# Optimization experiments

Measured on AMD Instinct MI355X. Metric: run time of the kernel, lower is better.

The kernel has to match this reference:

```python
import jax, jax.numpy as jnp
import numpy as np


def setup_inputs() -> dict:
    key = jax.random.key(0)
    k1, k2, k3, k4 = jax.random.split(key, 4)
    n, m = 4096, 1024  # n video frames, 1024-d features
    scale = 0.02
    return {
        "x": jax.random.normal(k1, (n, m), dtype=jnp.float32),
        "WQ": jax.random.normal(k2, (m, m), dtype=jnp.float32) * scale,  # torch Linear weight [out,in]
        "WK": jax.random.normal(k3, (m, m), dtype=jnp.float32) * scale,
        "WV": jax.random.normal(k4, (m, m), dtype=jnp.float32) * scale,
    }


def _quaternion_logits(q, k):
    """Hamilton-product attention logits: 4 tensors of shape [Lq, Lk]."""
    qr, qx, qy, qz = jnp.split(q, 4, axis=-1)
    kr, kx, ky, kz = jnp.split(k, 4, axis=-1)
    dot = lambda a, b: jnp.einsum('qd,kd->qk', a, b)
    r = dot(qr, kr) - dot(qx, kx) - dot(qy, ky) - dot(qz, kz)
    i = dot(qr, kx) + dot(qx, kr) + dot(qy, kz) - dot(qz, ky)
    j = dot(qr, ky) - dot(qx, kz) + dot(qy, kr) + dot(qz, kx)
    kk = dot(qr, kz) + dot(qx, ky) - dot(qy, kx) + dot(qz, kr)
    return [r, i, j, kk]


def reference(x, WQ, WK, WV):
    # QKV projections (torch Linear, no bias): y = x @ W.T
    Q = x @ WQ.T
    K = x @ WK.T
    V = x @ WV.T
    v_vals = jnp.split(V, 4, axis=-1)  # 4 chunks of depth d/4 (tensor2tensor quaternion attn)
    logits = _quaternion_logits(Q, K)
    outs = []
    w = None
    for l, v in zip(logits, v_vals):
        w = jax.nn.softmax(l, axis=-1)  # per-component softmax over keys
        outs.append(w @ v)
    y = jnp.concatenate(outs, axis=-1)  # [n, d]
    # original returns the attention weights from the last component (loop-leaked var)
    return y, w
```

## Files before the change

kernel.cpp:

```cpp
#include <hip/hip_runtime.h>
#include <cmath>

typedef __attribute__((ext_vector_type(8))) short short8;
typedef __attribute__((ext_vector_type(8))) unsigned short ushort8_t;
typedef __attribute__((ext_vector_type(8))) _Float16 half8;
typedef __attribute__((ext_vector_type(4))) float f32x4;
typedef unsigned short u16;

__device__ __forceinline__ u16 f2h(float f) {
    _Float16 h = (_Float16)f;
    return __builtin_bit_cast(u16, h);
}
__device__ __forceinline__ float h2f(u16 b) {
    return (float)__builtin_bit_cast(_Float16, b);
}

#define GLD16(g, l)                                                              \
    __builtin_amdgcn_global_load_lds(                                            \
        (const __attribute__((address_space(1))) unsigned int*)(g),              \
        (__attribute__((address_space(3))) unsigned int*)(l), 16, 0, 0)

#define MFMA_F16(a, b, c)                                                        \
    __builtin_amdgcn_mfma_f32_16x16x32_f16(                                      \
        __builtin_bit_cast(half8, (a)), __builtin_bit_cast(half8, (b)), (c), 0, 0, 0)
#define SBAR() asm volatile("s_barrier" ::: "memory")

__global__ __launch_bounds__(256) void to_h_all(
    const float* __restrict__ x, const float* __restrict__ WQ,
    const float* __restrict__ WK, const float* __restrict__ WV,
    u16* __restrict__ xh, u16* __restrict__ Wh)
{
    int bid = blockIdx.x;
    const float* src;
    u16* dst;
    int off;
    if (bid < 4096) { src = x; dst = xh; off = bid; }
    else {
        int j = bid - 4096;
        int wsel = j >> 10;
        off = j & 1023;
        src = wsel == 0 ? WQ : (wsel == 1 ? WK : WV);
        dst = Wh + (size_t)wsel * 1024 * 1024;
    }
    int idx = off * 256 + threadIdx.x;
    float4 v = reinterpret_cast<const float4*>(src)[idx];
    ushort4 h;
    h.x = f2h(v.x); h.y = f2h(v.y); h.z = f2h(v.z); h.w = f2h(v.w);
    reinterpret_cast<ushort4*>(dst)[idx] = h;
}

__global__ __launch_bounds__(512, 2) void logits8(
    const u16* __restrict__ A, const u16* __restrict__ B, const u16* __restrict__ Bneg,
    u16* __restrict__ P, float* __restrict__ pm, float* __restrict__ ps,
    int perm_packed, int sign_packed)
{
    constexpr int NT = 16;
    __shared__ u16 L[2][2][256 * 64];
    const int tid = threadIdx.x;
    const int l = tid & 63, w = tid >> 6;
    const int wr = w >> 2, wc = w & 3;
    const int lr = l & 15, lh = l >> 4;
    const int bid = (int)blockIdx.x;
    const int xcd = bid & 7, idx = bid >> 3;
    const int rowp = (xcd >> 1) * 4 + (idx >> 3);
    const int colp = (xcd & 1) * 8 + (idx & 7);
    const int row0 = rowp * 256, col0 = colp * 256;
    const int srow = l >> 3;
    const int scol = ((l & 7) ^ (l >> 3)) * 8;

    f32x4 acc[8][4] = {};

    auto stage = [&](int t) {
        int kA = t * 64;
        int ch = kA >> 8;
        int p = (perm_packed >> (2 * ch)) & 3;
        const u16* Bsrc = ((sign_packed >> ch) & 1) ? Bneg : B;
        int kB = (p << 8) + (kA & 255);
        int bf = t & 1;
        #pragma unroll
        for (int i = 0; i < 4; ++i) {
            int r0 = w * 32 + i * 8;
            GLD16(&A[(size_t)(row0 + r0 + srow) * 1024 + kA + scol], &L[bf][0][r0 * 64]);
        }
        #pragma unroll
        for (int i = 0; i < 4; ++i) {
            int r0 = w * 32 + i * 8;
            GLD16(&Bsrc[(size_t)(col0 + r0 + srow) * 1024 + kB + scol], &L[bf][1][r0 * 64]);
        }
    };
    auto readA = [&](int bf, int m, int kh) -> short8 {
        int row = wr * 128 + m * 16 + lr;
        int c = ((kh * 4 + lh) ^ (lr & 7)) * 8;
        return *reinterpret_cast<const short8*>(&L[bf][0][row * 64 + c]);
    };
    auto readB = [&](int bf, int n, int kh) -> short8 {
        int row = wc * 64 + n * 16 + lr;
        int c = ((kh * 4 + lh) ^ (lr & 7)) * 8;
        return *reinterpret_cast<const short8*>(&L[bf][1][row * 64 + c]);
    };

    stage(0);
    stage(1);
    asm volatile("s_waitcnt vmcnt(8)" ::: "memory");
    SBAR();

    #pragma unroll 2
    for (int t = 0; t < NT; ++t) {
        const int bf = t & 1;
        short8 am[4][2], bn[4][2];
        #pragma unroll
        for (int m = 0; m < 4; ++m) { am[m][0] = readA(bf, m, 0); am[m][1] = readA(bf, m, 1); }
        #pragma unroll
        for (int n = 0; n < 2; ++n) { bn[n][0] = readB(bf, n, 0); bn[n][1] = readB(bf, n, 1); }
        SBAR();
        __builtin_amdgcn_s_setprio(1);
        #pragma unroll
        for (int m = 0; m < 4; ++m)
            #pragma unroll
            for (int n = 0; n < 2; ++n) {
                acc[m][n] = MFMA_F16(am[m][0], bn[n][0], acc[m][n]);
                acc[m][n] = MFMA_F16(am[m][1], bn[n][1], acc[m][n]);
            }
        __builtin_amdgcn_s_setprio(0);
        SBAR();
        #pragma unroll
        for (int n = 2; n < 4; ++n) { bn[n][0] = readB(bf, n, 0); bn[n][1] = readB(bf, n, 1); }
        SBAR();
        __builtin_amdgcn_s_setprio(1);
        #pragma unroll
        for (int m = 0; m < 4; ++m)
            #pragma unroll
            for (int n = 2; n < 4; ++n) {
                acc[m][n] = MFMA_F16(am[m][0], bn[n][0], acc[m][n]);
                acc[m][n] = MFMA_F16(am[m][1], bn[n][1], acc[m][n]);
            }
        __builtin_amdgcn_s_setprio(0);
        SBAR();
        #pragma unroll
        for (int m = 0; m < 4; ++m) { am[m][0] = readA(bf, 4 + m, 0); am[m][1] = readA(bf, 4 + m, 1); }
        SBAR();
        __builtin_amdgcn_s_setprio(1);
        #pragma unroll
        for (int m = 0; m < 4; ++m)
            #pragma unroll
            for (int n = 2; n < 4; ++n) {
                acc[4 + m][n] = MFMA_F16(am[m][0], bn[n][0], acc[4 + m][n]);
                acc[4 + m][n] = MFMA_F16(am[m][1], bn[n][1], acc[4 + m][n]);
            }
        __builtin_amdgcn_s_setprio(0);
        SBAR();
        if (t + 2 < NT) stage(t + 2);
        SBAR();
        __builtin_amdgcn_s_setprio(1);
        #pragma unroll
        for (int m = 0; m < 4; ++m)
            #pragma unroll
            for (int n = 0; n < 2; ++n) {
                acc[4 + m][n] = MFMA_F16(am[m][0], bn[n][0], acc[4 + m][n]);
                acc[4 + m][n] = MFMA_F16(am[m][1], bn[n][1], acc[4 + m][n]);
            }
        __builtin_amdgcn_s_setprio(0);
        if (t + 2 < NT) { asm volatile("s_waitcnt vmcnt(8)" ::: "memory"); }
        else           { asm volatile("s_waitcnt vmcnt(0)" ::: "memory"); }
        SBAR();
    }

    const int tcol = (col0 >> 6) + wc;
    float* T = reinterpret_cast<float*>(&L[0][0][0]) + w * 1088;
    const int rq = l >> 2;
    const int cq = l & 3;
    #pragma unroll
    for (int m = 0; m < 8; ++m) {
        #pragma unroll
        for (int n = 0; n < 4; ++n)
            #pragma unroll
            for (int j = 0; j < 4; ++j)
                T[(lh * 4 + j) * 68 + n * 16 + lr] = acc[m][n][j];
        float vals[16];
        #pragma unroll
        for (int q = 0; q < 4; ++q) {
            f32x4 v4 = *reinterpret_cast<const f32x4*>(&T[rq * 68 + cq * 16 + q * 4]);
            vals[q * 4 + 0] = v4[0]; vals[q * 4 + 1] = v4[1];
            vals[q * 4 + 2] = v4[2]; vals[q * 4 + 3] = v4[3];
        }
        float mx = vals[0];
        #pragma unroll
        for (int c = 1; c < 16; ++c) mx = fmaxf(mx, vals[c]);
        mx = fmaxf(mx, __shfl_xor(mx, 1, 64));
        mx = fmaxf(mx, __shfl_xor(mx, 2, 64));
        float e[16];
        float s = 0.f;
        #pragma unroll
        for (int c = 0; c < 16; ++c) { e[c] = expf(vals[c] - mx); s += e[c]; }
        s += __shfl_xor(s, 1, 64);
        s += __shfl_xor(s, 2, 64);
        int row = row0 + wr * 128 + m * 16 + rq;
        if (cq == 0) {
            pm[(size_t)row * 64 + tcol] = mx;
            ps[(size_t)row * 64 + tcol] = s;
        }
        ushort8_t d0, d1;
        #pragma unroll
        for (int c = 0; c < 8; ++c) d0[c] = f2h(e[c]);
        #pragma unroll
        for (int c = 0; c < 8; ++c) d1[c] = f2h(e[c + 8]);
        size_t go = (size_t)row * 4096 + col0 + wc * 64 + cq * 16;
        *reinterpret_cast<ushort8_t*>(&P[go]) = d0;
        *reinterpret_cast<ushort8_t*>(&P[go + 8]) = d1;
    }
}

__global__ __launch_bounds__(512, 2) void qkv8(
    const u16* __restrict__ A, const u16* __restrict__ B,
    u16* __restrict__ Qh, u16* __restrict__ Kh, u16* __restrict__ Khn,
    u16* __restrict__ Vt)
{
    constexpr int NT = 16;
    __shared__ u16 L[2][2][256 * 64];
    const int tid = threadIdx.x;
    const int l = tid & 63, w = tid >> 6;
    const int wr = w >> 2, wc = w & 3;
    const int lr = l & 15, lh = l >> 4;
    const int bid = (int)blockIdx.x;
    const int wgid = (bid & 7) * 24 + (bid >> 3);
    const int row0 = (wgid / 12) * 256, col0 = (wgid % 12) * 256;
    const int srow = l >> 3;
    const int scol = ((l & 7) ^ (l >> 3)) * 8;

    f32x4 acc[8][4] = {};

    auto stage = [&](int t) {
        int k0 = t * 64;
        int bf = t & 1;
        #pragma unroll
        for (int i = 0; i < 4; ++i) {
            int r0 = w * 32 + i * 8;
            GLD16(&A[(size_t)(row0 + r0 + srow) * 1024 + k0 + scol], &L[bf][0][r0 * 64]);
        }
        #pragma unroll
        for (int i = 0; i < 4; ++i) {
            int r0 = w * 32 + i * 8;
            GLD16(&B[(size_t)(col0 + r0 + srow) * 1024 + k0 + scol], &L[bf][1][r0 * 64]);
        }
    };
    auto readA = [&](int bf, int m, int kh) -> short8 {
        int row = wr * 128 + m * 16 + lr;
        int c = ((kh * 4 + lh) ^ (lr & 7)) * 8;
        return *reinterpret_cast<const short8*>(&L[bf][0][row * 64 + c]);
    };
    auto readB = [&](int bf, int n, int kh) -> short8 {
        int row = wc * 64 + n * 16 + lr;
        int c = ((kh * 4 + lh) ^ (lr & 7)) * 8;
        return *reinterpret_cast<const short8*>(&L[bf][1][row * 64 + c]);
    };

    stage(0);
    stage(1);
    asm volatile("s_waitcnt vmcnt(8)" ::: "memory");
    SBAR();

    #pragma unroll 2
    for (int t = 0; t < NT; ++t) {
        const int bf = t & 1;
        short8 am[4][2], bn[4][2];
        #pragma unroll
        for (int m = 0; m < 4; ++m) { am[m][0] = readA(bf, m, 0); am[m][1] = readA(bf, m, 1); }
        #pragma unroll
        for (int n = 0; n < 2; ++n) { bn[n][0] = readB(bf, n, 0); bn[n][1] = readB(bf, n, 1); }
        SBAR();
        __builtin_amdgcn_s_setprio(1);
        #pragma unroll
        for (int m = 0; m < 4; ++m)
            #pragma unroll
            for (int n = 0; n < 2; ++n) {
                acc[m][n] = MFMA_F16(am[m][0], bn[n][0], acc[m][n]);
                acc[m][n] = MFMA_F16(am[m][1], bn[n][1], acc[m][n]);
            }
        __builtin_amdgcn_s_setprio(0);
        SBAR();
        #pragma unroll
        for (int n = 2; n < 4; ++n) { bn[n][0] = readB(bf, n, 0); bn[n][1] = readB(bf, n, 1); }
        SBAR();
        __builtin_amdgcn_s_setprio(1);
        #pragma unroll
        for (int m = 0; m < 4; ++m)
            #pragma unroll
            for (int n = 2; n < 4; ++n) {
                acc[m][n] = MFMA_F16(am[m][0], bn[n][0], acc[m][n]);
                acc[m][n] = MFMA_F16(am[m][1], bn[n][1], acc[m][n]);
            }
        __builtin_amdgcn_s_setprio(0);
        SBAR();
        #pragma unroll
        for (int m = 0; m < 4; ++m) { am[m][0] = readA(bf, 4 + m, 0); am[m][1] = readA(bf, 4 + m, 1); }
        SBAR();
        __builtin_amdgcn_s_setprio(1);
        #pragma unroll
        for (int m = 0; m < 4; ++m)
            #pragma unroll
            for (int n = 2; n < 4; ++n) {
                acc[4 + m][n] = MFMA_F16(am[m][0], bn[n][0], acc[4 + m][n]);
                acc[4 + m][n] = MFMA_F16(am[m][1], bn[n][1], acc[4 + m][n]);
            }
        __builtin_amdgcn_s_setprio(0);
        SBAR();
        if (t + 2 < NT) stage(t + 2);
        SBAR();
        __builtin_amdgcn_s_setprio(1);
        #pragma unroll
        for (int m = 0; m < 4; ++m)
            #pragma unroll
            for (int n = 0; n < 2; ++n) {
                acc[4 + m][n] = MFMA_F16(am[m][0], bn[n][0], acc[4 + m][n]);
                acc[4 + m][n] = MFMA_F16(am[m][1], bn[n][1], acc[4 + m][n]);
            }
        __builtin_amdgcn_s_setprio(0);
        if (t + 2 < NT) { asm volatile("s_waitcnt vmcnt(8)" ::: "memory"); }
        else           { asm volatile("s_waitcnt vmcnt(0)" ::: "memory"); }
        SBAR();
    }

    const int mode = col0 >> 10;
    #pragma unroll
    for (int m = 0; m < 8; ++m)
        #pragma unroll
        for (int n = 0; n < 4; ++n) {
            int gr = row0 + wr * 128 + m * 16 + lh * 4;
            int gc = col0 + wc * 64 + n * 16 + lr;
            int gcl = gc & 1023;
            f32x4 v = acc[m][n];
            if (mode == 0) {
                #pragma unroll
                for (int j = 0; j < 4; ++j)
                    Qh[(size_t)(gr + j) * 1024 + gcl] = f2h(v[j]);
            } else if (mode == 1) {
                #pragma unroll
                for (int j = 0; j < 4; ++j) {
                    u16 h = f2h(v[j]);
                    size_t o = (size_t)(gr + j) * 1024 + gcl;
                    Kh[o] = h; Khn[o] = h ^ 0x8000;
                }
            } else {
                ushort4 o;
                o.x = f2h(v[0]); o.y = f2h(v[1]); o.z = f2h(v[2]); o.w = f2h(v[3]);
                *reinterpret_cast<ushort4*>(&Vt[(size_t)gcl * 4096 + gr]) = o;
            }
        }
}

template<bool WRITE_W>
__global__ __launch_bounds__(256) void pv_fused(
    const u16* __restrict__ P, float* __restrict__ Wout,
    const u16* __restrict__ Vt, const float* __restrict__ pm,
    const float* __restrict__ ps, u16* __restrict__ ypart, int c256)
{
    __shared__ u16 As[64 * 64];
    __shared__ u16 Bs[256 * 64];
    __shared__ float Red[64][4];
    __shared__ float Ms[64], Is[64];
    const int tid = threadIdx.x;
    const int l = tid & 63, w = tid >> 6;
    const int lr = l & 15, lh = l >> 4;
    const int kc = blockIdx.x;
    const int row0 = blockIdx.y * 64;
    const int kbase = kc * 512;
    const int srow = l >> 3, scol = ((l & 7) ^ (l >> 3)) * 8;

    {
        int row = tid & 63, part = tid >> 6;
        const float* pmr = &pm[(size_t)(row0 + row) * 64 + part * 16];
        const float* psr = &ps[(size_t)(row0 + row) * 64 + part * 16];
        float M = -INFINITY;
        #pragma unroll
        for (int i = 0; i < 16; ++i) M = fmaxf(M, pmr[i]);
        Red[row][part] = M;
        __syncthreads();
        float Mg = fmaxf(fmaxf(Red[row][0], Red[row][1]),
                         fmaxf(Red[row][2], Red[row][3]));
        float S = 0.f;
        #pragma unroll
        for (int i = 0; i < 16; ++i) S += psr[i] * expf(pmr[i] - Mg);
        __syncthreads();
        Red[row][part] = S;
        __syncthreads();
        if (tid < 64) {
            float Sg = Red[tid][0] + Red[tid][1] + Red[tid][2] + Red[tid][3];
            Ms[tid] = Mg;
            Is[tid] = 1.0f / Sg;
        }
        __syncthreads();
    }

    float Mr[4], Ir[4];
    #pragma unroll
    for (int i = 0; i < 4; ++i) { int r = (tid >> 4) + i * 16; Mr[i] = Ms[r]; Ir[i] = Is[r]; }

    f32x4 acc[4][4] = {};

    for (int kt = 0; kt < 8; ++kt) {
        const int tcol = kc * 8 + kt;
        __syncthreads();
        #pragma unroll
        for (int i = 0; i < 4; ++i) {
            int idx = tid + i * 256;
            int r = idx >> 4, s4 = idx & 15;
            float alpha = expf(pm[(size_t)(row0 + r) * 64 + tcol] - Mr[i]) * Ir[i];
            size_t ga = (size_t)(row0 + r) * 4096 + kbase + kt * 64 + s4 * 4;
            ushort4 dv = *reinterpret_cast<const ushort4*>(&P[ga]);
            float e0 = h2f(dv.x) * alpha;
            float e1 = h2f(dv.y) * alpha;
            float e2 = h2f(dv.z) * alpha;
            float e3 = h2f(dv.w) * alpha;
            if (WRITE_W)
                *reinterpret_cast<float4*>(&Wout[ga]) = make_float4(e0, e1, e2, e3);
            ushort4 h;
            h.x = f2h(e0); h.y = f2h(e1); h.z = f2h(e2); h.w = f2h(e3);
            int dst = ((s4 >> 1) ^ (r & 7)) * 8 + (s4 & 1) * 4;
            *reinterpret_cast<ushort4*>(&As[r * 64 + dst]) = h;
        }
        #pragma unroll
        for (int i = 0; i < 8; ++i) {
            int r0 = w * 64 + i * 8;
            GLD16(&Vt[(size_t)(c256 + r0 + srow) * 4096 + kbase + kt * 64 + scol],
                  &Bs[r0 * 64]);
        }
        __syncthreads();
        #pragma unroll
        for (int kh = 0; kh < 2; ++kh) {
            short8 af[4], bfv[4];
            #pragma unroll
            for (int m = 0; m < 4; ++m)
                af[m] = *reinterpret_cast<const short8*>(
                    &As[(m * 16 + lr) * 64 + ((kh * 4 + lh) ^ (lr & 7)) * 8]);
            #pragma unroll
            for (int n = 0; n < 4; ++n)
                bfv[n] = *reinterpret_cast<const short8*>(
                    &Bs[(w * 64 + n * 16 + lr) * 64 + ((kh * 4 + lh) ^ (lr & 7)) * 8]);
            #pragma unroll
            for (int m = 0; m < 4; ++m)
                #pragma unroll
                for (int n = 0; n < 4; ++n)
                    acc[m][n] = MFMA_F16(af[m], bfv[n], acc[m][n]);
        }
    }

    #pragma unroll
    for (int m = 0; m < 4; ++m)
        #pragma unroll
        for (int n = 0; n < 4; ++n) {
            int rr = m * 16 + lh * 4;
            int col = w * 64 + n * 16 + lr;
            #pragma unroll
            for (int j = 0; j < 4; ++j)
                ypart[((size_t)kc * 4096 + row0 + rr + j) * 256 + col] = f2h(acc[m][n][j]);
        }
}

__global__ __launch_bounds__(256) void reduce_y(const u16* __restrict__ ypart,
                                                float* __restrict__ y, int c256)
{
    int idx = blockIdx.x * 256 + threadIdx.x;
    int r = idx >> 6, c4 = (idx & 63) * 4;
    float s0 = 0.f, s1 = 0.f, s2 = 0.f, s3 = 0.f;
    #pragma unroll
    for (int kc = 0; kc < 8; ++kc) {
        ushort4 p = *reinterpret_cast<const ushort4*>(
            &ypart[((size_t)kc * 4096 + r) * 256 + c4]);
        s0 += h2f(p.x); s1 += h2f(p.y); s2 += h2f(p.z); s3 += h2f(p.w);
    }
    *reinterpret_cast<float4*>(&y[(size_t)r * 1024 + c256 + c4]) =
        make_float4(s0, s1, s2, s3);
}

extern "C" void kernel_launch(void* const* d_in, const int* in_sizes, int n_in,
                              void* d_out, int out_size, void* d_ws, size_t ws_size,
                              hipStream_t stream)
{
    const int n = 4096, d = 1024;
    const float* x  = (const float*)d_in[0];
    const float* WQ = (const float*)d_in[1];
    const float* WK = (const float*)d_in[2];
    const float* WV = (const float*)d_in[3];

    float* y = (float*)d_out;
    float* wout = y + (size_t)n * d;

    u16* P    = (u16*)d_ws;
    u16* xh   = P;
    u16* Wh   = P + (size_t)n * 1024;
    u16* Qh   = P + (size_t)n * 4096;
    u16* Kh   = Qh  + (size_t)n * 1024;
    u16* Khn  = Kh  + (size_t)n * 1024;
    u16* Vt   = Khn + (size_t)n * 1024;
    u16* ypart = Vt + (size_t)d * 4096;
    float* pm = (float*)(ypart + (size_t)8 * n * 256);
    float* ps = pm + (size_t)n * 64;

    to_h_all<<<7168, 256, 0, stream>>>(x, WQ, WK, WV, xh, Wh);

    qkv8<<<192, 512, 0, stream>>>(xh, Wh, Qh, Kh, Khn, Vt);

    const int permv[4] = {0xE4, 0xB1, 0x4E, 0x1B};
    const int signv[4] = {0x0E, 0x08, 0x02, 0x04};

    for (int c = 0; c < 4; ++c) {
        logits8<<<256, 512, 0, stream>>>(Qh, Kh, Khn, P, pm, ps, permv[c], signv[c]);
        if (c == 3)
            pv_fused<true><<<dim3(8, 64), 256, 0, stream>>>(P, wout, Vt, pm, ps, ypart, c * 256);
        else
            pv_fused<false><<<dim3(8, 64), 256, 0, stream>>>(P, wout, Vt, pm, ps, ypart, c * 256);
        reduce_y<<<1024, 256, 0, stream>>>(ypart, y, c * 256);
    }
}
```

Before: 332.2 us.

## Compute all four quaternion logit components in one kernel sharing Q/K tiles

Replaces four separate logits8 launches (one per quaternion component, each reloading permuted Q/K chunks and a pre-negated K copy) with a single logits4 kernel. Each 128x128 tile loads all four Q and K sub-blocks once and produces all four component logits by combining blocks and flipping signs in registers. This drops the Khn buffer and the repeated Q/K loads. In exchange it holds four accumulator sets per wave with one block per CU, has no double-buffered pipelining, and writes all four P matrices (4x32MB) to workspace before the PV passes, which costs extra memory traffic and cache locality.

After: 418.6 us. +26.0%, slower.

```diff
diff --git a/kernel.cpp b/kernel.cpp
--- a/kernel.cpp
+++ b/kernel.cpp
@@ -5,6 +5,7 @@
 typedef __attribute__((ext_vector_type(8))) unsigned short ushort8_t;
 typedef __attribute__((ext_vector_type(8))) _Float16 half8;
 typedef __attribute__((ext_vector_type(4))) float f32x4;
+typedef __attribute__((ext_vector_type(4))) unsigned int u32x4;
 typedef unsigned short u16;
 
 __device__ __forceinline__ u16 f2h(float f) {
@@ -13,6 +14,11 @@
 }
 __device__ __forceinline__ float h2f(u16 b) {
     return (float)__builtin_bit_cast(_Float16, b);
+}
+__device__ __forceinline__ short8 neg16(short8 v) {
+    u32x4 u = __builtin_bit_cast(u32x4, v);
+    u ^= 0x80008000u;
+    return __builtin_bit_cast(short8, u);
 }
 
 #define GLD16(g, l)                                                              \
@@ -49,10 +55,135 @@
     reinterpret_cast<ushort4*>(dst)[idx] = h;
 }
 
-__global__ __launch_bounds__(512, 2) void logits8(
-    const u16* __restrict__ A, const u16* __restrict__ B, const u16* __restrict__ Bneg,
-    u16* __restrict__ P, float* __restrict__ pm, float* __restrict__ ps,
-    int perm_packed, int sign_packed)
+__global__ __launch_bounds__(512, 1) void logits4(
+    const u16* __restrict__ Qh, const u16* __restrict__ Kh,
+    u16* __restrict__ P4, float* __restrict__ pm4, float* __restrict__ ps4)
+{
+    __shared__ u16 L[8][128 * 64];
+    const int tid = threadIdx.x;
+    const int l = tid & 63, w = tid >> 6;
+    const int wr = w >> 1, wc = w & 1;
+    const int lr = l & 15, lh = l >> 4;
+    const int bid = (int)blockIdx.x;
+    const int xcd = bid & 7, idx = bid >> 3;
+    const int rowp = (xcd >> 1) * 8 + (idx >> 4);
+    const int colp = (xcd & 1) * 16 + (idx & 15);
+    const int row0 = rowp * 128, col0 = colp * 128;
+    const int srow = l >> 3;
+    const int scol = ((l & 7) ^ (l >> 3)) * 8;
+
+    f32x4 acc[4][2][4] = {};
+
+    for (int s = 0; s < 4; ++s) {
+        __syncthreads();
+        #pragma unroll
+        for (int a = 0; a < 4; ++a) {
+            int kq = a * 256 + s * 64;
+            #pragma unroll
+            for (int i = 0; i < 2; ++i) {
+                int r0 = w * 16 + i * 8;
+                GLD16(&Qh[(size_t)(row0 + r0 + srow) * 1024 + kq + scol],
+                      &L[a][r0 * 64]);
+                GLD16(&Kh[(size_t)(col0 + r0 + srow) * 1024 + kq + scol],
+                      &L[4 + a][r0 * 64]);
+            }
+        }
+        __syncthreads();
+
+        __builtin_amdgcn_s_setprio(1);
+        #pragma unroll
+        for (int b = 0; b < 4; ++b) {
+            short8 bn[4][2];
+            #pragma unroll
+            for (int n = 0; n < 4; ++n)
+                #pragma unroll
+                for (int kh = 0; kh < 2; ++kh)
+                    bn[n][kh] = *reinterpret_cast<const short8*>(
+                        &L[4 + b][(wc * 64 + n * 16 + lr) * 64 +
+                                  ((kh * 4 + lh) ^ (lr & 7)) * 8]);
+            #pragma unroll
+            for (int a = 0; a < 4; ++a) {
+                const int c = a ^ b;
+                constexpr int SG[4] = {0x0E, 0x08, 0x02, 0x04};
+                const bool sgn = (SG[c] >> a) & 1;
+                short8 am[2][2];
+                #pragma unroll
+                for (int m = 0; m < 2; ++m)
+                    #pragma unroll
+                    for (int kh = 0; kh < 2; ++kh) {
+                        am[m][kh] = *reinterpret_cast<const short8*>(
+                            &L[a][(wr * 32 + m * 16 + lr) * 64 +
+                                  ((kh * 4 + lh) ^ (lr & 7)) * 8]);
+                        if (sgn) am[m][kh] = neg16(am[m][kh]);
+                    }
+                #pragma unroll
+                for (int m = 0; m < 2; ++m)
+                    #pragma unroll
+                    for (int n = 0; n < 4; ++n) {
+                        acc[c][m][n] = MFMA_F16(am[m][0], bn[n][0], acc[c][m][n]);
+                        acc[c][m][n] = MFMA_F16(am[m][1], bn[n][1], acc[c][m][n]);
+                    }
+            }
+        }
+        __builtin_amdgcn_s_setprio(0);
+    }
+    __syncthreads();
+
+    const int tcol = (col0 >> 6) + wc;
+    float* T = reinterpret_cast<float*>(&L[0][0]) + w * 1088;
+    const int rq = l >> 2;
+    const int cq = l & 3;
+    #pragma unroll
+    for (int c = 0; c < 4; ++c) {
+        u16* P = P4 + (size_t)c * 4096 * 4096;
+        float* pm = pm4 + (size_t)c * 4096 * 64;
+        float* ps = ps4 + (size_t)c * 4096 * 64;
+        #pragma unroll
+        for (int m = 0; m < 2; ++m) {
+            #pragma unroll
+            for (int n = 0; n < 4; ++n)
+                #pragma unroll
+                for (int j = 0; j < 4; ++j)
+                    T[(lh * 4 + j) * 68 + n * 16 + lr] = acc[c][m][n][j];
+            float vals[16];
+            #pragma unroll
+            for (int q = 0; q < 4; ++q) {
+                f32x4 v4 = *reinterpret_cast<const f32x4*>(
+                    &T[rq * 68 + cq * 16 + q * 4]);
+                vals[q * 4 + 0] = v4[0]; vals[q * 4 + 1] = v4[1];
+                vals[q * 4 + 2] = v4[2]; vals[q * 4 + 3] = v4[3];
+            }
+            float mx = vals[0];
+            #pragma unroll
+            for (int k = 1; k < 16; ++k) mx = fmaxf(mx, vals[k]);
+            mx = fmaxf(mx, __shfl_xor(mx, 1, 64));
+            mx = fmaxf(mx, __shfl_xor(mx, 2, 64));
+            float e[16];
+            float sm = 0.f;
+            #pragma unroll
+            for (int k = 0; k < 16; ++k) { e[k] = expf(vals[k] - mx); sm += e[k]; }
+            sm += __shfl_xor(sm, 1, 64);
+            sm += __shfl_xor(sm, 2, 64);
+            int row = row0 + wr * 32 + m * 16 + rq;
+            if (cq == 0) {
+                pm[(size_t)row * 64 + tcol] = mx;
+                ps[(size_t)row * 64 + tcol] = sm;
+            }
+            ushort8_t d0, d1;
+            #pragma unroll
+            for (int k = 0; k < 8; ++k) d0[k] = f2h(e[k]);
+            #pragma unroll
+            for (int k = 0; k < 8; ++k) d1[k] = f2h(e[k + 8]);
+            size_t go = (size_t)row * 4096 + col0 + wc * 64 + cq * 16;
+            *reinterpret_cast<ushort8_t*>(&P[go]) = d0;
+            *reinterpret_cast<ushort8_t*>(&P[go + 8]) = d1;
+        }
+    }
+}
+
+__global__ __launch_bounds__(512, 2) void qkv8(
+    const u16* __restrict__ A, const u16* __restrict__ B,
+    u16* __restrict__ Qh, u16* __restrict__ Kh, u16* __restrict__ Vt)
 {
     constexpr int NT = 16;
     __shared__ u16 L[2][2][256 * 64];
@@ -61,31 +192,25 @@
     const int wr = w >> 2, wc = w & 3;
     const int lr = l & 15, lh = l >> 4;
     const int bid = (int)blockIdx.x;
-    const int xcd = bid & 7, idx = bid >> 3;
-    const int rowp = (xcd >> 1) * 4 + (idx >> 3);
-    const int colp = (xcd & 1) * 8 + (idx & 7);
-    const int row0 = rowp * 256, col0 = colp * 256;
+    const int wgid = (bid & 7) * 24 + (bid >> 3);
+    const int row0 = (wgid / 12) * 256, col0 = (wgid % 12) * 256;
     const int srow = l >> 3;
     const int scol = ((l & 7) ^ (l >> 3)) * 8;
 
     f32x4 acc[8][4] = {};
 
     auto stage = [&](int t) {
-        int kA = t * 64;
-        int ch = kA >> 8;
-        int p = (perm_packed >> (2 * ch)) & 3;
-        const u16* Bsrc = ((sign_packed >> ch) & 1) ? Bneg : B;
-        int kB = (p << 8) + (kA & 255);
+        int k0 = t * 64;
         int bf = t & 1;
         #pragma unroll
         for (int i = 0; i < 4; ++i) {
             int r0 = w * 32 + i * 8;
-            GLD16(&A[(size_t)(row0 + r0 + srow) * 1024 + kA + scol], &L[bf][0][r0 * 64]);
+            GLD16(&A[(size_t)(row0 + r0 + srow) * 1024 + k0 + scol], &L[bf][0][r0 * 64]);
         }
         #pragma unroll
         for (int i = 0; i < 4; ++i) {
             int r0 = w * 32 + i * 8;
-            GLD16(&Bsrc[(size_t)(col0 + r0 + srow) * 1024 + kB + scol], &L[bf][1][r0 * 64]);
+            GLD16(&B[(size_t)(col0 + r0 + srow) * 1024 + k0 + scol], &L[bf][1][r0 * 64]);
         }
     };
     auto readA = [&](int bf, int m, int kh) -> short8 {
@@ -165,161 +290,6 @@
         SBAR();
     }
 
-    const int tcol = (col0 >> 6) + wc;
-    float* T = reinterpret_cast<float*>(&L[0][0][0]) + w * 1088;
-    const int rq = l >> 2;
-    const int cq = l & 3;
-    #pragma unroll
-    for (int m = 0; m < 8; ++m) {
-        #pragma unroll
-        for (int n = 0; n < 4; ++n)
-            #pragma unroll
-            for (int j = 0; j < 4; ++j)
-                T[(lh * 4 + j) * 68 + n * 16 + lr] = acc[m][n][j];
-        float vals[16];
-        #pragma unroll
-        for (int q = 0; q < 4; ++q) {
-            f32x4 v4 = *reinterpret_cast<const f32x4*>(&T[rq * 68 + cq * 16 + q * 4]);
-            vals[q * 4 + 0] = v4[0]; vals[q * 4 + 1] = v4[1];
-            vals[q * 4 + 2] = v4[2]; vals[q * 4 + 3] = v4[3];
-        }
-        float mx = vals[0];
-        #pragma unroll
-        for (int c = 1; c < 16; ++c) mx = fmaxf(mx, vals[c]);
-        mx = fmaxf(mx, __shfl_xor(mx, 1, 64));
-        mx = fmaxf(mx, __shfl_xor(mx, 2, 64));
-        float e[16];
-        float s = 0.f;
-        #pragma unroll
-        for (int c = 0; c < 16; ++c) { e[c] = expf(vals[c] - mx); s += e[c]; }
-        s += __shfl_xor(s, 1, 64);
-        s += __shfl_xor(s, 2, 64);
-        int row = row0 + wr * 128 + m * 16 + rq;
-        if (cq == 0) {
-            pm[(size_t)row * 64 + tcol] = mx;
-            ps[(size_t)row * 64 + tcol] = s;
-        }
-        ushort8_t d0, d1;
-        #pragma unroll
-        for (int c = 0; c < 8; ++c) d0[c] = f2h(e[c]);
-        #pragma unroll
-        for (int c = 0; c < 8; ++c) d1[c] = f2h(e[c + 8]);
-        size_t go = (size_t)row * 4096 + col0 + wc * 64 + cq * 16;
-        *reinterpret_cast<ushort8_t*>(&P[go]) = d0;
-        *reinterpret_cast<ushort8_t*>(&P[go + 8]) = d1;
-    }
-}
-
-__global__ __launch_bounds__(512, 2) void qkv8(
-    const u16* __restrict__ A, const u16* __restrict__ B,
-    u16* __restrict__ Qh, u16* __restrict__ Kh, u16* __restrict__ Khn,
-    u16* __restrict__ Vt)
-{
-    constexpr int NT = 16;
-    __shared__ u16 L[2][2][256 * 64];
-    const int tid = threadIdx.x;
-    const int l = tid & 63, w = tid >> 6;
-    const int wr = w >> 2, wc = w & 3;
-    const int lr = l & 15, lh = l >> 4;
-    const int bid = (int)blockIdx.x;
-    const int wgid = (bid & 7) * 24 + (bid >> 3);
-    const int row0 = (wgid / 12) * 256, col0 = (wgid % 12) * 256;
-    const int srow = l >> 3;
-    const int scol = ((l & 7) ^ (l >> 3)) * 8;
-
-    f32x4 acc[8][4] = {};
-
-    auto stage = [&](int t) {
-        int k0 = t * 64;
-        int bf = t & 1;
-        #pragma unroll
-        for (int i = 0; i < 4; ++i) {
-            int r0 = w * 32 + i * 8;
-            GLD16(&A[(size_t)(row0 + r0 + srow) * 1024 + k0 + scol], &L[bf][0][r0 * 64]);
-        }
-        #pragma unroll
-        for (int i = 0; i < 4; ++i) {
-            int r0 = w * 32 + i * 8;
-            GLD16(&B[(size_t)(col0 + r0 + srow) * 1024 + k0 + scol], &L[bf][1][r0 * 64]);
-        }
-    };
-    auto readA = [&](int bf, int m, int kh) -> short8 {
-        int row = wr * 128 + m * 16 + lr;
-        int c = ((kh * 4 + lh) ^ (lr & 7)) * 8;
-        return *reinterpret_cast<const short8*>(&L[bf][0][row * 64 + c]);
-    };
-    auto readB = [&](int bf, int n, int kh) -> short8 {
-        int row = wc * 64 + n * 16 + lr;
-        int c = ((kh * 4 + lh) ^ (lr & 7)) * 8;
-        return *reinterpret_cast<const short8*>(&L[bf][1][row * 64 + c]);
-    };
-
-    stage(0);
-    stage(1);
-    asm volatile("s_waitcnt vmcnt(8)" ::: "memory");
-    SBAR();
-
-    #pragma unroll 2
-    for (int t = 0; t < NT; ++t) {
-        const int bf = t & 1;
-        short8 am[4][2], bn[4][2];
-        #pragma unroll
-        for (int m = 0; m < 4; ++m) { am[m][0] = readA(bf, m, 0); am[m][1] = readA(bf, m, 1); }
-        #pragma unroll
-        for (int n = 0; n < 2; ++n) { bn[n][0] = readB(bf, n, 0); bn[n][1] = readB(bf, n, 1); }
-        SBAR();
-        __builtin_amdgcn_s_setprio(1);
-        #pragma unroll
-        for (int m = 0; m < 4; ++m)
-            #pragma unroll
-            for (int n = 0; n < 2; ++n) {
-                acc[m][n] = MFMA_F16(am[m][0], bn[n][0], acc[m][n]);
-                acc[m][n] = MFMA_F16(am[m][1], bn[n][1], acc[m][n]);
-            }
-        __builtin_amdgcn_s_setprio(0);
-        SBAR();
-        #pragma unroll
-        for (int n = 2; n < 4; ++n) { bn[n][0] = readB(bf, n, 0); bn[n][1] = readB(bf, n, 1); }
-        SBAR();
-        __builtin_amdgcn_s_setprio(1);
-        #pragma unroll
-        for (int m = 0; m < 4; ++m)
-            #pragma unroll
-            for (int n = 2; n < 4; ++n) {
-                acc[m][n] = MFMA_F16(am[m][0], bn[n][0], acc[m][n]);
-                acc[m][n] = MFMA_F16(am[m][1], bn[n][1], acc[m][n]);
-            }
-        __builtin_amdgcn_s_setprio(0);
-        SBAR();
-        #pragma unroll
-        for (int m = 0; m < 4; ++m) { am[m][0] = readA(bf, 4 + m, 0); am[m][1] = readA(bf, 4 + m, 1); }
-        SBAR();
-        __builtin_amdgcn_s_setprio(1);
-        #pragma unroll
-        for (int m = 0; m < 4; ++m)
-            #pragma unroll
-            for (int n = 2; n < 4; ++n) {
-                acc[4 + m][n] = MFMA_F16(am[m][0], bn[n][0], acc[4 + m][n]);
-                acc[4 + m][n] = MFMA_F16(am[m][1], bn[n][1], acc[4 + m][n]);
-            }
-        __builtin_amdgcn_s_setprio(0);
-        SBAR();
-        if (t + 2 < NT) stage(t + 2);
-        SBAR();
-        __builtin_amdgcn_s_setprio(1);
-        #pragma unroll
-        for (int m = 0; m < 4; ++m)
-            #pragma unroll
-            for (int n = 0; n < 2; ++n) {
-                acc[4 + m][n] = MFMA_F16(am[m][0], bn[n][0], acc[4 + m][n]);
-                acc[4 + m][n] = MFMA_F16(am[m][1], bn[n][1], acc[4 + m][n]);
-            }
-        __builtin_amdgcn_s_setprio(0);
-        if (t + 2 < NT) { asm volatile("s_waitcnt vmcnt(8)" ::: "memory"); }
-        else           { asm volatile("s_waitcnt vmcnt(0)" ::: "memory"); }
-        SBAR();
-    }
-
     const int mode = col0 >> 10;
     #pragma unroll
     for (int m = 0; m < 8; ++m)
@@ -335,11 +305,8 @@
                     Qh[(size_t)(gr + j) * 1024 + gcl] = f2h(v[j]);
             } else if (mode == 1) {
                 #pragma unroll
-                for (int j = 0; j < 4; ++j) {
-                    u16 h = f2h(v[j]);
-                    size_t o = (size_t)(gr + j) * 1024 + gcl;
-                    Kh[o] = h; Khn[o] = h ^ 0x8000;
-                }
+                for (int j = 0; j < 4; ++j)
+                    Kh[(size_t)(gr + j) * 1024 + gcl] = f2h(v[j]);
             } else {
                 ushort4 o;
                 o.x = f2h(v[0]); o.y = f2h(v[1]); o.z = f2h(v[2]); o.w = f2h(v[3]);
@@ -477,6 +444,7 @@
                               hipStream_t stream)
 {
     const int n = 4096, d = 1024;
+    const size_t NN = (size_t)n * n;
     const float* x  = (const float*)d_in[0];
     const float* WQ = (const float*)d_in[1];
     const float* WK = (const float*)d_in[2];
@@ -485,30 +453,31 @@
     float* y = (float*)d_out;
     float* wout = y + (size_t)n * d;
 
-    u16* P    = (u16*)d_ws;
-    u16* xh   = P;
-    u16* Wh   = P + (size_t)n * 1024;
-    u16* Qh   = P + (size_t)n * 4096;
-    u16* Kh   = Qh  + (size_t)n * 1024;
-    u16* Khn  = Kh  + (size_t)n * 1024;
-    u16* Vt   = Khn + (size_t)n * 1024;
+    u16* P4   = (u16*)d_ws;
+    u16* xh   = P4;
+    u16* Wh   = P4 + (size_t)n * 1024;
+    u16* Qh   = P4 + 4 * NN;
+    u16* Kh   = Qh + (size_t)n * 1024;
+    u16* Vt   = Kh + (size_t)n * 1024;
     u16* ypart = Vt + (size_t)d * 4096;
-    float* pm = (float*)(ypart + (size_t)8 * n * 256);
-    float* ps = pm + (size_t)n * 64;
+    float* pm4 = (float*)(ypart + (size_t)8 * n * 256);
+    float* ps4 = pm4 + 4 * (size_t)n * 64;
 
     to_h_all<<<7168, 256, 0, stream>>>(x, WQ, WK, WV, xh, Wh);
-
-    qkv8<<<192, 512, 0, stream>>>(xh, Wh, Qh, Kh, Khn, Vt);
-
-    const int permv[4] = {0xE4, 0xB1, 0x4E, 0x1B};
-    const int signv[4] = {0x0E, 0x08, 0x02, 0x04};
+    qkv8<<<192, 512, 0, stream>>>(xh, Wh, Qh, Kh, Vt);
+
+    logits4<<<1024, 512, 0, stream>>>(Qh, Kh, P4, pm4, ps4);
 
     for (int c = 0; c < 4; ++c) {
-        logits8<<<256, 512, 0, stream>>>(Qh, Kh, Khn, P, pm, ps, permv[c], signv[c]);
+        const u16* Pc = P4 + (size_t)c * NN;
+        const float* pmc = pm4 + (size_t)c * n * 64;
+        const float* psc = ps4 + (size_t)c * n * 64;
         if (c == 3)
-            pv_fused<true><<<dim3(8, 64), 256, 0, stream>>>(P, wout, Vt, pm, ps, ypart, c * 256);
+            pv_fused<true><<<dim3(8, 64), 256, 0, stream>>>(
+                Pc, wout, Vt, pmc, psc, ypart, c * 256);
         else
-            pv_fused<false><<<dim3(8, 64), 256, 0, stream>>>(P, wout, Vt, pm, ps, ypart, c * 256);
+            pv_fused<false><<<dim3(8, 64), 256, 0, stream>>>(
+                Pc, wout, Vt, pmc, psc, ypart, c * 256);
         reduce_y<<<1024, 256, 0, stream>>>(ypart, y, c * 256);
     }
 }
```
